# Optimization experiments

Measured on AMD Instinct MI355X. Metric: run time of the kernel, lower is better.

The kernel has to match this reference:

```python
import jax, jax.numpy as jnp
import numpy as np

NUM_NODES = 80000
NUM_EDGES = 1280000
NUM_GRAPHS = 512
IN_DIM = 64
HID = 64
NUM_CLASSES = 10


def setup_inputs() -> dict:
    key = jax.random.key(0)
    ks = jax.random.split(key, 16)
    x = jax.random.normal(ks[0], (NUM_NODES, IN_DIM), dtype=jnp.float32)
    edge_index = jax.random.randint(ks[1], (2, NUM_EDGES), 0, NUM_NODES, dtype=jnp.int64)
    batch = jnp.sort(jax.random.randint(ks[2], (NUM_NODES,), 0, NUM_GRAPHS, dtype=jnp.int64))

    def glorot(k, shape):
        fan_in, fan_out = shape[1], shape[0]
        lim = jnp.sqrt(6.0 / (fan_in + fan_out))
        return jax.random.uniform(k, shape, dtype=jnp.float32, minval=-lim, maxval=lim)

    inp = {
        "x": x,
        "edge_index": edge_index,
        "batch": batch,
        # GraphConv layer 1: lin_rel (with bias) applied to aggregated neighbors, lin_root (no bias)
        "w_rel1": glorot(ks[3], (HID, IN_DIM)),
        "b_rel1": jnp.zeros((HID,), dtype=jnp.float32),
        "w_root1": glorot(ks[4], (HID, IN_DIM)),
        # layer 2
        "w_rel2": glorot(ks[5], (HID, HID)),
        "b_rel2": jnp.zeros((HID,), dtype=jnp.float32),
        "w_root2": glorot(ks[6], (HID, HID)),
        # layer 3
        "w_rel3": glorot(ks[7], (HID, HID)),
        "b_rel3": jnp.zeros((HID,), dtype=jnp.float32),
        "w_root3": glorot(ks[8], (HID, HID)),
        # final linear head
        "w_lin": glorot(ks[9], (NUM_CLASSES, HID)),
        "b_lin": jnp.zeros((NUM_CLASSES,), dtype=jnp.float32),
    }
    return inp


def _graph_conv(x, src, dst, w_rel, b_rel, w_root):
    # PyG GraphConv with aggr='add': out_i = W_rel @ (sum_{j in N(i)} x_j) + b_rel + W_root @ x_i
    agg = jax.ops.segment_sum(x[src], dst, num_segments=NUM_NODES)  # [N, d_in]
    return agg @ w_rel.T + b_rel + x @ w_root.T


def reference(x, edge_index, batch,
              w_rel1, b_rel1, w_root1,
              w_rel2, b_rel2, w_root2,
              w_rel3, b_rel3, w_root3,
              w_lin, b_lin):
    src, dst = edge_index[0], edge_index[1]
    h = jax.nn.relu(_graph_conv(x, src, dst, w_rel1, b_rel1, w_root1))
    h = jax.nn.relu(_graph_conv(h, src, dst, w_rel2, b_rel2, w_root2))
    h = _graph_conv(h, src, dst, w_rel3, b_rel3, w_root3)
    # global_mean_pool over graph ids
    sums = jax.ops.segment_sum(h, batch, num_segments=NUM_GRAPHS)          # [G, HID]
    counts = jax.ops.segment_sum(jnp.ones((h.shape[0],), h.dtype), batch, num_segments=NUM_GRAPHS)
    pooled = sums / jnp.maximum(counts, 1.0)[:, None]
    # dropout p=0.5 is identity at inference (training=False)
    return pooled @ w_lin.T + b_lin  # [G, NUM_CLASSES]
```

## Files before the change

### kernel.cpp

```cpp
#include <hip/hip_runtime.h>

#define N_NODES  80000
#define N_EDGES  1280000
#define N_GRAPHS 512
#define DIM      64
#define NCLS     10

#define ETILE    2048
#define NTILE    625
#define NCB      313
#define CBPAD    320

typedef _Float16 half8f __attribute__((ext_vector_type(8)));
typedef float float4f __attribute__((ext_vector_type(4)));

static __device__ __forceinline__ unsigned short f2h(float f) {
    _Float16 h = (_Float16)f;
    return __builtin_bit_cast(unsigned short, h);
}
static __device__ __forceinline__ float h_lo(unsigned v) {
    return (float)__builtin_bit_cast(_Float16, (unsigned short)(v & 0xFFFF));
}
static __device__ __forceinline__ float h_hi(unsigned v) {
    return (float)__builtin_bit_cast(_Float16, (unsigned short)(v >> 16));
}

__global__ __launch_bounds__(256) void k_histprep(const int* __restrict__ ei,
        const float* __restrict__ x,
        const float* __restrict__ wr1, const float* __restrict__ wo1,
        const float* __restrict__ wr2, const float* __restrict__ wo2,
        int* __restrict__ hmat, unsigned short* __restrict__ xb,
        unsigned short* __restrict__ wf) {
    __shared__ int hist[NCB];
    int bid = blockIdx.x, t = threadIdx.x;
    if (bid < NTILE) {
        int tile = bid;
        for (int i = t; i < NCB; i += 256) hist[i] = 0;
        __syncthreads();
        int base = tile * ETILE;
        int end = base + ETILE;
        for (int i = base + t; i < end; i += 256)
            atomicAdd(&hist[ei[N_EDGES + i] >> 8], 1);
        __syncthreads();
        for (int i = t; i < NCB; i += 256) hmat[tile * CBPAD + i] = hist[i];
        return;
    }
    int pb = bid - NTILE;
    if (pb < 5000) {
        int i = pb * 256 + t;
        float4 v = ((const float4*)x)[i];
        ushort4 o;
        o.x = f2h(v.x); o.y = f2h(v.y); o.z = f2h(v.z); o.w = f2h(v.w);
        ((ushort4*)xb)[i] = o;
    } else {
        int idx = (pb - 5000) * 256 + t;
        int j = idx & 7, lane = (idx >> 3) & 63;
        int ks = (idx >> 9) & 3, nt = (idx >> 11) & 3, l = idx >> 13;
        int k = ks * 32 + ((lane >> 4) & 3) * 8 + j;
        int n = nt * 16 + (lane & 15);
        const float* wr = (l == 0) ? wr1 : wr2;
        const float* wo = (l == 0) ? wo1 : wo2;
        float val = (k < 64) ? wr[n * 64 + k] : wo[n * 64 + (k - 64)];
        wf[idx] = f2h(val);
    }
}

__global__ __launch_bounds__(256) void k_scanT(const int* __restrict__ hmat,
        int* __restrict__ obase, int* __restrict__ btot) {
    __shared__ int sa[256], sb[256];
    int b = blockIdx.x, t = threadIdx.x;
    int j0 = 3 * t;
    int l0 = (j0     < NTILE) ? hmat[(j0    ) * CBPAD + b] : 0;
    int l1 = (j0 + 1 < NTILE) ? hmat[(j0 + 1) * CBPAD + b] : 0;
    int l2 = (j0 + 2 < NTILE) ? hmat[(j0 + 2) * CBPAD + b] : 0;
    int s = l0 + l1 + l2;
    sa[t] = s; __syncthreads();
    int* sp = sa; int* dp = sb;
    for (int off = 1; off < 256; off <<= 1) {
        dp[t] = sp[t] + ((t >= off) ? sp[t - off] : 0);
        __syncthreads();
        int* tmp = sp; sp = dp; dp = tmp;
    }
    int ex = sp[t] - s;
    if (j0     < NTILE) obase[(j0    ) * CBPAD + b] = ex;
    if (j0 + 1 < NTILE) obase[(j0 + 1) * CBPAD + b] = ex + l0;
    if (j0 + 2 < NTILE) obase[(j0 + 2) * CBPAD + b] = ex + l0 + l1;
    if (t == 255) btot[b] = sp[255];
}

__global__ __launch_bounds__(256) void k_scatter2(const int* __restrict__ ei,
        const int* __restrict__ obase, const int* __restrict__ btot,
        int* __restrict__ ebuf) {
    __shared__ int sa[256], sb[256];
    __shared__ int bbase[NCB];
    __shared__ int cur[NCB];
    int tile = blockIdx.x, t = threadIdx.x;
    int l0 = (2 * t     < NCB) ? btot[2 * t]     : 0;
    int l1 = (2 * t + 1 < NCB) ? btot[2 * t + 1] : 0;
    int s = l0 + l1;
    sa[t] = s; __syncthreads();
    int* sp = sa; int* dp = sb;
    for (int off = 1; off < 256; off <<= 1) {
        dp[t] = sp[t] + ((t >= off) ? sp[t - off] : 0);
        __syncthreads();
        int* tmp = sp; sp = dp; dp = tmp;
    }
    int ex = sp[t] - s;
    if (2 * t     < NCB) bbase[2 * t]     = ex;
    if (2 * t + 1 < NCB) bbase[2 * t + 1] = ex + l0;
    __syncthreads();
    for (int i = t; i < NCB; i += 256)
        cur[i] = bbase[i] + obase[tile * CBPAD + i];
    __syncthreads();
    int base = tile * ETILE;
    int end = base + ETILE;
    for (int i = base + t; i < end; i += 256) {
        int sv = ei[i], d = ei[N_EDGES + i];
        int p = atomicAdd(&cur[d >> 8], 1);
        ebuf[p] = sv | ((d & 255) << 17);
    }
}

__global__ __launch_bounds__(256) void k_csr2(const int* __restrict__ ebuf,
        const int* __restrict__ btot, int* __restrict__ rowptr,
        int* __restrict__ col) {
    __shared__ int sa[256], sb[256];
    __shared__ int bbase[NCB];
    __shared__ int cnt[256], cur[256];
    int b = blockIdx.x, t = threadIdx.x;
    int l0 = (2 * t     < NCB) ? btot[2 * t]     : 0;
    int l1 = (2 * t + 1 < NCB) ? btot[2 * t + 1] : 0;
    int sm = l0 + l1;
    sa[t] = sm; __syncthreads();
    int* sp = sa; int* dp = sb;
    for (int off = 1; off < 256; off <<= 1) {
        dp[t] = sp[t] + ((t >= off) ? sp[t - off] : 0);
        __syncthreads();
        int* tmp = sp; sp = dp; dp = tmp;
    }
    int ex = sp[t] - sm;
    if (2 * t     < NCB) bbase[2 * t]     = ex;
    if (2 * t + 1 < NCB) bbase[2 * t + 1] = ex + l0;
    cnt[t] = 0;
    __syncthreads();
    int s = bbase[b];
    int e = s + btot[b];
    for (int i = s + t; i < e; i += 256) atomicAdd(&cnt[ebuf[i] >> 17], 1);
    __syncthreads();
    int c = cnt[t];
    sa[t] = c; __syncthreads();
    sp = sa; dp = sb;
    for (int off = 1; off < 256; off <<= 1) {
        dp[t] = sp[t] + ((t >= off) ? sp[t - off] : 0);
        __syncthreads();
        int* tmp = sp; sp = dp; dp = tmp;
    }
    int rowbase = s + sp[t] - c;
    cur[t] = rowbase;
    int node = b * 256 + t;
    if (node <= N_NODES) rowptr[node] = rowbase;
    __syncthreads();
    for (int i = s + t; i < e; i += 256) {
        int pk = ebuf[i];
        int p = atomicAdd(&cur[pk >> 17], 1);
        col[p] = pk & 0x1FFFF;
    }
}

__global__ __launch_bounds__(256) void k_gatherlin(
        const unsigned short* __restrict__ Xin,
        const int* __restrict__ rowptr, const int* __restrict__ col,
        const unsigned short* __restrict__ wf, const float* __restrict__ bias,
        unsigned short* __restrict__ out, int relu) {
    __shared__ uint4 sAgg[64][9];
    const half8f* Xq = (const half8f*)Xin;
    int t = threadIdx.x, w = t >> 6, lane = t & 63;
    int e = lane >> 3, c = lane & 7;
    int nb = blockIdx.x * 64 + w * 16;
    int rp = (lane <= 16) ? rowptr[nb + lane] : 0;
    for (int n = 0; n < 16; ++n) {
        int start = __shfl(rp, n), end = __shfl(rp, n + 1);
        half8f acc = {};
        int base = start;
        for (; base + 16 <= end; base += 16) {
            int i0 = col[base + e];
            int i1 = col[base + 8 + e];
            half8f v0 = Xq[(size_t)i0 * 8 + c];
            half8f v1 = Xq[(size_t)i1 * 8 + c];
            acc = acc + v0;
            acc = acc + v1;
        }
        for (; base + 8 <= end; base += 8) {
            int i0 = col[base + e];
            acc = acc + Xq[(size_t)i0 * 8 + c];
        }
        int r = end - base;
        if (e < r) {
            int i0 = col[base + e];
            acc = acc + Xq[(size_t)i0 * 8 + c];
        }
#pragma unroll
        for (int off = 8; off < 64; off <<= 1) {
            uint4 au = __builtin_bit_cast(uint4, acc);
            uint4 bu;
            bu.x = __shfl_xor(au.x, off); bu.y = __shfl_xor(au.y, off);
            bu.z = __shfl_xor(au.z, off); bu.w = __shfl_xor(au.w, off);
            acc = acc + __builtin_bit_cast(half8f, bu);
        }
        if (e == 0) sAgg[w * 16 + n][c] = __builtin_bit_cast(uint4, acc);
    }
    int quad = lane >> 4, l15 = lane & 15;
    int m = nb + l15;
    half8f a0 = *(const half8f*)&sAgg[w * 16 + l15][quad];
    half8f a1 = *(const half8f*)&sAgg[w * 16 + l15][4 + quad];
    const half8f* xr = (const half8f*)(Xin + (size_t)m * 64);
    half8f a2 = xr[quad];
    half8f a3 = xr[4 + quad];
    int orow = nb + quad * 4;
#pragma unroll
    for (int nt = 0; nt < 4; ++nt) {
        const half8f* wp = (const half8f*)(wf + ((size_t)(nt * 4) * 64 + lane) * 8);
        half8f b0 = wp[0];
        half8f b1 = wp[64];
        half8f b2 = wp[128];
        half8f b3 = wp[192];
        float4f acc = {0.f, 0.f, 0.f, 0.f};
        acc = __builtin_amdgcn_mfma_f32_16x16x32_f16(a0, b0, acc, 0, 0, 0);
        acc = __builtin_amdgcn_mfma_f32_16x16x32_f16(a1, b1, acc, 0, 0, 0);
        acc = __builtin_amdgcn_mfma_f32_16x16x32_f16(a2, b2, acc, 0, 0, 0);
        acc = __builtin_amdgcn_mfma_f32_16x16x32_f16(a3, b3, acc, 0, 0, 0);
        float bi = bias[nt * 16 + l15];
#pragma unroll
        for (int r = 0; r < 4; ++r) {
            float v = acc[r] + bi;
            if (relu) v = fmaxf(v, 0.f);
            out[(size_t)(orow + r) * 64 + nt * 16 + l15] = f2h(v);
        }
    }
}

static __device__ __forceinline__ int lowerb(const int* a, int n, int key) {
    int lo = 0, hi = n;
    while (lo < hi) { int mid = (lo + hi) >> 1; if (a[mid] < key) lo = mid + 1; else hi = mid; }
    return lo;
}

__global__ __launch_bounds__(256) void k_gsum(const unsigned short* __restrict__ h2,
        const int* __restrict__ rowptr, const int* __restrict__ col,
        const int* __restrict__ batch, float* __restrict__ S4) {
    __shared__ float red1[8][64];
    __shared__ float red2[8][64];
    const unsigned* Xu = (const unsigned*)h2;
    int g = blockIdx.x >> 2, part = blockIdx.x & 3;
    int t = threadIdx.x;
    int hw = t >> 5, c = t & 31;
    int ns = lowerb(batch, N_NODES, g);
    int ne = lowerb(batch, N_NODES, g + 1);
    int a0 = ns + (int)(((long long)(ne - ns) * part) >> 2);
    int a1 = ns + (int)(((long long)(ne - ns) * (part + 1)) >> 2);
    int es = rowptr[a0], ee = rowptr[a1];
    float alo = 0.f, ahi = 0.f;
    int nfull = (ee - es) >> 7;
    int e0 = es + hw * 16;
    for (int b = 0; b < nfull; ++b, e0 += 128) {
        unsigned v[16];
#pragma unroll
        for (int j = 0; j < 16; ++j)
            v[j] = Xu[(size_t)col[e0 + j] * 32 + c];
#pragma unroll
        for (int j = 0; j < 16; ++j) { alo += h_lo(v[j]); ahi += h_hi(v[j]); }
    }
    for (int e = es + nfull * 128 + hw; e < ee; e += 8) {
        unsigned v = Xu[(size_t)col[e] * 32 + c];
        alo += h_lo(v); ahi += h_hi(v);
    }
    float blo = 0.f, bhi = 0.f;
    for (int i = a0 + hw; i < a1; i += 8) {
        unsigned v = Xu[(size_t)i * 32 + c];
        blo += h_lo(v); bhi += h_hi(v);
    }
    red1[hw][2 * c] = alo; red1[hw][2 * c + 1] = ahi;
    red2[hw][2 * c] = blo; red2[hw][2 * c + 1] = bhi;
    __syncthreads();
    if (t < 64) {
        float v = 0.f;
#pragma unroll
        for (int s = 0; s < 8; ++s) v += red1[s][t];
        S4[(size_t)blockIdx.x * 128 + t] = v;
    } else if (t < 128) {
        float v = 0.f;
#pragma unroll
        for (int s = 0; s < 8; ++s) v += red2[s][t - 64];
        S4[(size_t)blockIdx.x * 128 + 64 + (t - 64)] = v;
    }
}

__global__ __launch_bounds__(64) void k_head2(const float* __restrict__ S4,
        const int* __restrict__ batch,
        const float* __restrict__ wr3, const float* __restrict__ wo3,
        const float* __restrict__ b3,
        const float* __restrict__ wlin, const float* __restrict__ blin,
        float* __restrict__ out) {
    __shared__ float s1[64], s2[64], pl[64];
    int g = blockIdx.x, t = threadIdx.x;
    int ns = lowerb(batch, N_NODES, g);
    int ne = lowerb(batch, N_NODES, g + 1);
    float inv = 1.f / (float)((ne > ns) ? (ne - ns) : 1);
    const float* Sg = S4 + (size_t)g * 4 * 128;
    s1[t] = (Sg[t]       + Sg[128 + t]       + Sg[256 + t]       + Sg[384 + t]) * inv;
    s2[t] = (Sg[64 + t]  + Sg[192 + t]       + Sg[320 + t]       + Sg[448 + t]) * inv;
    __syncthreads();
    float acc = b3[t];
    for (int k = 0; k < 64; ++k)
        acc += s1[k] * wr3[t * 64 + k] + s2[k] * wo3[t * 64 + k];
    pl[t] = acc;
    __syncthreads();
    float myout = 0.f;
    for (int cls = 0; cls < NCLS; ++cls) {
        float vv = pl[t] * wlin[cls * 64 + t];
        for (int off = 32; off > 0; off >>= 1) vv += __shfl_xor(vv, off);
        if (t == cls) myout = vv + blin[cls];
    }
    if (t < NCLS) out[g * NCLS + t] = myout;
}

extern "C" void kernel_launch(void* const* d_in, const int* in_sizes, int n_in,
                              void* d_out, int out_size, void* d_ws, size_t ws_size,
                              hipStream_t stream) {
    const float* x     = (const float*)d_in[0];
    const int*   ei    = (const int*)d_in[1];
    const int*   batch = (const int*)d_in[2];
    const float* wr1 = (const float*)d_in[3];
    const float* b1  = (const float*)d_in[4];
    const float* wo1 = (const float*)d_in[5];
    const float* wr2 = (const float*)d_in[6];
    const float* b2  = (const float*)d_in[7];
    const float* wo2 = (const float*)d_in[8];
    const float* wr3 = (const float*)d_in[9];
    const float* b3  = (const float*)d_in[10];
    const float* wo3 = (const float*)d_in[11];
    const float* wlin = (const float*)d_in[12];
    const float* blin = (const float*)d_in[13];
    float* out = (float*)d_out;

    char* p = (char*)d_ws;
    auto alloc = [&](size_t bytes) { char* r = p; p += (bytes + 255) & ~(size_t)255; return r; };
    int*   rowptr  = (int*)alloc((N_NODES + 1) * sizeof(int));
    int*   hmat    = (int*)alloc((size_t)NTILE * CBPAD * sizeof(int));
    int*   obase   = (int*)alloc((size_t)NTILE * CBPAD * sizeof(int));
    int*   btot    = (int*)alloc(CBPAD * sizeof(int));
    int*   ebuf    = (int*)alloc((size_t)N_EDGES * sizeof(int));
    int*   col     = (int*)alloc((size_t)N_EDGES * sizeof(int));
    unsigned short* wf  = (unsigned short*)alloc(2 * 8192 * sizeof(unsigned short));
    unsigned short* xbf = (unsigned short*)alloc((size_t)N_NODES * 64 * 2);
    unsigned short* hA  = (unsigned short*)alloc((size_t)N_NODES * 64 * 2);
    unsigned short* hB  = (unsigned short*)alloc((size_t)N_NODES * 64 * 2);
    float* S4      = (float*)alloc((size_t)N_GRAPHS * 4 * 128 * sizeof(float));

    k_histprep<<<NTILE + 5064, 256, 0, stream>>>(ei, x, wr1, wo1, wr2, wo2,
                                                 hmat, xbf, wf);
    k_scanT   <<<NCB,   256, 0, stream>>>(hmat, obase, btot);
    k_scatter2<<<NTILE, 256, 0, stream>>>(ei, obase, btot, ebuf);
    k_csr2    <<<NCB,   256, 0, stream>>>(ebuf, btot, rowptr, col);

    k_gatherlin<<<N_NODES / 64, 256, 0, stream>>>(xbf, rowptr, col, wf,        b1, hA, 1);
    k_gatherlin<<<N_NODES / 64, 256, 0, stream>>>(hA,  rowptr, col, wf + 8192, b2, hB, 1);

    k_gsum <<<N_GRAPHS * 4, 256, 0, stream>>>(hB, rowptr, col, batch, S4);
    k_head2<<<N_GRAPHS,     64,  0, stream>>>(S4, batch, wr3, wo3, b3, wlin, blin, out);
}
```

Before: 238.7 us.

## Use finer CSR buckets, single bucket-base scan, and vectorized gsum gathers

Bucket width for the CSR build drops from 256 to 128 nodes, so more blocks work on smaller buckets in the scan and CSR kernels. The global bucket prefix sum, which every scatter and CSR block used to recompute, now runs once in a new single-block kernel that writes bucketbase and rowptr[N]. The graph-sum kernel switches to 16-byte uint4 gathers with two loads in flight per iteration and a wave-shuffle reduction in place of 32-bit loads. The cost is one extra kernel launch and a larger histogram matrix.

```diff
diff --git a/kernel.cpp b/kernel.cpp
--- a/kernel.cpp
+++ b/kernel.cpp
@@ -8,8 +8,9 @@
 
 #define ETILE    2048
 #define NTILE    625
-#define NCB      313
-#define CBPAD    320
+#define NCB      625
+#define BSH      7
+#define HPAD     640
 
 typedef _Float16 half8f __attribute__((ext_vector_type(8)));
 typedef float float4f __attribute__((ext_vector_type(4)));
@@ -40,9 +41,9 @@
         int base = tile * ETILE;
         int end = base + ETILE;
         for (int i = base + t; i < end; i += 256)
-            atomicAdd(&hist[ei[N_EDGES + i] >> 8], 1);
-        __syncthreads();
-        for (int i = t; i < NCB; i += 256) hmat[tile * CBPAD + i] = hist[i];
+            atomicAdd(&hist[ei[N_EDGES + i] >> BSH], 1);
+        __syncthreads();
+        for (int i = t; i < NCB; i += 256) hmat[tile * HPAD + i] = hist[i];
         return;
     }
     int pb = bid - NTILE;
@@ -70,9 +71,9 @@
     __shared__ int sa[256], sb[256];
     int b = blockIdx.x, t = threadIdx.x;
     int j0 = 3 * t;
-    int l0 = (j0     < NTILE) ? hmat[(j0    ) * CBPAD + b] : 0;
-    int l1 = (j0 + 1 < NTILE) ? hmat[(j0 + 1) * CBPAD + b] : 0;
-    int l2 = (j0 + 2 < NTILE) ? hmat[(j0 + 2) * CBPAD + b] : 0;
+    int l0 = (j0     < NTILE) ? hmat[(j0    ) * HPAD + b] : 0;
+    int l1 = (j0 + 1 < NTILE) ? hmat[(j0 + 1) * HPAD + b] : 0;
+    int l2 = (j0 + 2 < NTILE) ? hmat[(j0 + 2) * HPAD + b] : 0;
     int s = l0 + l1 + l2;
     sa[t] = s; __syncthreads();
     int* sp = sa; int* dp = sb;
@@ -82,22 +83,23 @@
         int* tmp = sp; sp = dp; dp = tmp;
     }
     int ex = sp[t] - s;
-    if (j0     < NTILE) obase[(j0    ) * CBPAD + b] = ex;
-    if (j0 + 1 < NTILE) obase[(j0 + 1) * CBPAD + b] = ex + l0;
-    if (j0 + 2 < NTILE) obase[(j0 + 2) * CBPAD + b] = ex + l0 + l1;
+    if (j0     < NTILE) obase[(j0    ) * HPAD + b] = ex;
+    if (j0 + 1 < NTILE) obase[(j0 + 1) * HPAD + b] = ex + l0;
+    if (j0 + 2 < NTILE) obase[(j0 + 2) * HPAD + b] = ex + l0 + l1;
     if (t == 255) btot[b] = sp[255];
 }
 
-__global__ __launch_bounds__(256) void k_scatter2(const int* __restrict__ ei,
-        const int* __restrict__ obase, const int* __restrict__ btot,
-        int* __restrict__ ebuf) {
+__global__ __launch_bounds__(256) void k_scanB(const int* __restrict__ btot,
+        int* __restrict__ bucketbase, int* __restrict__ rowptr) {
     __shared__ int sa[256], sb[256];
-    __shared__ int bbase[NCB];
-    __shared__ int cur[NCB];
-    int tile = blockIdx.x, t = threadIdx.x;
-    int l0 = (2 * t     < NCB) ? btot[2 * t]     : 0;
-    int l1 = (2 * t + 1 < NCB) ? btot[2 * t + 1] : 0;
-    int s = l0 + l1;
+    int t = threadIdx.x;
+    int b0 = t * 5;
+    int v0 = (b0     < NCB) ? btot[b0]     : 0;
+    int v1 = (b0 + 1 < NCB) ? btot[b0 + 1] : 0;
+    int v2 = (b0 + 2 < NCB) ? btot[b0 + 2] : 0;
+    int v3 = (b0 + 3 < NCB) ? btot[b0 + 3] : 0;
+    int v4 = (b0 + 4 < NCB) ? btot[b0 + 4] : 0;
+    int s = v0 + v1 + v2 + v3 + v4;
     sa[t] = s; __syncthreads();
     int* sp = sa; int* dp = sb;
     for (int off = 1; off < 256; off <<= 1) {
@@ -106,59 +108,55 @@
         int* tmp = sp; sp = dp; dp = tmp;
     }
     int ex = sp[t] - s;
-    if (2 * t     < NCB) bbase[2 * t]     = ex;
-    if (2 * t + 1 < NCB) bbase[2 * t + 1] = ex + l0;
-    __syncthreads();
+    if (b0     < NCB) bucketbase[b0]     = ex;
+    if (b0 + 1 < NCB) bucketbase[b0 + 1] = ex + v0;
+    if (b0 + 2 < NCB) bucketbase[b0 + 2] = ex + v0 + v1;
+    if (b0 + 3 < NCB) bucketbase[b0 + 3] = ex + v0 + v1 + v2;
+    if (b0 + 4 < NCB) bucketbase[b0 + 4] = ex + v0 + v1 + v2 + v3;
+    if (t == 0) { bucketbase[NCB] = N_EDGES; rowptr[N_NODES] = N_EDGES; }
+}
+
+__global__ __launch_bounds__(256) void k_scatter2(const int* __restrict__ ei,
+        const int* __restrict__ obase, const int* __restrict__ bucketbase,
+        int* __restrict__ ebuf) {
+    __shared__ int cur[NCB];
+    int tile = blockIdx.x, t = threadIdx.x;
     for (int i = t; i < NCB; i += 256)
-        cur[i] = bbase[i] + obase[tile * CBPAD + i];
+        cur[i] = bucketbase[i] + obase[tile * HPAD + i];
     __syncthreads();
     int base = tile * ETILE;
     int end = base + ETILE;
     for (int i = base + t; i < end; i += 256) {
         int sv = ei[i], d = ei[N_EDGES + i];
-        int p = atomicAdd(&cur[d >> 8], 1);
-        ebuf[p] = sv | ((d & 255) << 17);
+        int p = atomicAdd(&cur[d >> BSH], 1);
+        ebuf[p] = sv | ((d & 127) << 17);
     }
 }
 
 __global__ __launch_bounds__(256) void k_csr2(const int* __restrict__ ebuf,
-        const int* __restrict__ btot, int* __restrict__ rowptr,
+        const int* __restrict__ bucketbase, int* __restrict__ rowptr,
         int* __restrict__ col) {
-    __shared__ int sa[256], sb[256];
-    __shared__ int bbase[NCB];
-    __shared__ int cnt[256], cur[256];
+    __shared__ int cnt[128], cur[128];
+    __shared__ int sa[128], sb[128];
     int b = blockIdx.x, t = threadIdx.x;
-    int l0 = (2 * t     < NCB) ? btot[2 * t]     : 0;
-    int l1 = (2 * t + 1 < NCB) ? btot[2 * t + 1] : 0;
-    int sm = l0 + l1;
-    sa[t] = sm; __syncthreads();
+    int s = bucketbase[b], e = bucketbase[b + 1];
+    if (t < 128) cnt[t] = 0;
+    __syncthreads();
+    for (int i = s + t; i < e; i += 256) atomicAdd(&cnt[ebuf[i] >> 17], 1);
+    __syncthreads();
+    if (t < 128) sa[t] = cnt[t];
+    __syncthreads();
     int* sp = sa; int* dp = sb;
-    for (int off = 1; off < 256; off <<= 1) {
-        dp[t] = sp[t] + ((t >= off) ? sp[t - off] : 0);
+    for (int off = 1; off < 128; off <<= 1) {
+        if (t < 128) dp[t] = sp[t] + ((t >= off) ? sp[t - off] : 0);
         __syncthreads();
         int* tmp = sp; sp = dp; dp = tmp;
     }
-    int ex = sp[t] - sm;
-    if (2 * t     < NCB) bbase[2 * t]     = ex;
-    if (2 * t + 1 < NCB) bbase[2 * t + 1] = ex + l0;
-    cnt[t] = 0;
-    __syncthreads();
-    int s = bbase[b];
-    int e = s + btot[b];
-    for (int i = s + t; i < e; i += 256) atomicAdd(&cnt[ebuf[i] >> 17], 1);
-    __syncthreads();
-    int c = cnt[t];
-    sa[t] = c; __syncthreads();
-    sp = sa; dp = sb;
-    for (int off = 1; off < 256; off <<= 1) {
-        dp[t] = sp[t] + ((t >= off) ? sp[t - off] : 0);
-        __syncthreads();
-        int* tmp = sp; sp = dp; dp = tmp;
-    }
-    int rowbase = s + sp[t] - c;
-    cur[t] = rowbase;
-    int node = b * 256 + t;
-    if (node <= N_NODES) rowptr[node] = rowbase;
+    if (t < 128) {
+        int rowbase = s + sp[t] - cnt[t];
+        cur[t] = rowbase;
+        rowptr[b * 128 + t] = rowbase;
+    }
     __syncthreads();
     for (int i = s + t; i < e; i += 256) {
         int pk = ebuf[i];
@@ -248,50 +246,68 @@
 __global__ __launch_bounds__(256) void k_gsum(const unsigned short* __restrict__ h2,
         const int* __restrict__ rowptr, const int* __restrict__ col,
         const int* __restrict__ batch, float* __restrict__ S4) {
-    __shared__ float red1[8][64];
-    __shared__ float red2[8][64];
-    const unsigned* Xu = (const unsigned*)h2;
+    __shared__ float red1[4][64];
+    __shared__ float red2[4][64];
+    const uint4* Xq = (const uint4*)h2;
     int g = blockIdx.x >> 2, part = blockIdx.x & 3;
-    int t = threadIdx.x;
-    int hw = t >> 5, c = t & 31;
+    int t = threadIdx.x, w = t >> 6, lane = t & 63;
+    int e = lane >> 3, c = lane & 7;
     int ns = lowerb(batch, N_NODES, g);
     int ne = lowerb(batch, N_NODES, g + 1);
     int a0 = ns + (int)(((long long)(ne - ns) * part) >> 2);
     int a1 = ns + (int)(((long long)(ne - ns) * (part + 1)) >> 2);
     int es = rowptr[a0], ee = rowptr[a1];
-    float alo = 0.f, ahi = 0.f;
-    int nfull = (ee - es) >> 7;
-    int e0 = es + hw * 16;
-    for (int b = 0; b < nfull; ++b, e0 += 128) {
-        unsigned v[16];
-#pragma unroll
-        for (int j = 0; j < 16; ++j)
-            v[j] = Xu[(size_t)col[e0 + j] * 32 + c];
-#pragma unroll
-        for (int j = 0; j < 16; ++j) { alo += h_lo(v[j]); ahi += h_hi(v[j]); }
-    }
-    for (int e = es + nfull * 128 + hw; e < ee; e += 8) {
-        unsigned v = Xu[(size_t)col[e] * 32 + c];
-        alo += h_lo(v); ahi += h_hi(v);
-    }
-    float blo = 0.f, bhi = 0.f;
-    for (int i = a0 + hw; i < a1; i += 8) {
-        unsigned v = Xu[(size_t)i * 32 + c];
-        blo += h_lo(v); bhi += h_hi(v);
-    }
-    red1[hw][2 * c] = alo; red1[hw][2 * c + 1] = ahi;
-    red2[hw][2 * c] = blo; red2[hw][2 * c + 1] = bhi;
+    float acc[8] = {0.f, 0.f, 0.f, 0.f, 0.f, 0.f, 0.f, 0.f};
+    int idx = es + w * 8 + e;
+    for (; idx + 32 < ee; idx += 64) {
+        int i0 = col[idx];
+        int i1 = col[idx + 32];
+        uint4 v0 = Xq[(size_t)i0 * 8 + c];
+        uint4 v1 = Xq[(size_t)i1 * 8 + c];
+        acc[0] += h_lo(v0.x) + h_lo(v1.x); acc[1] += h_hi(v0.x) + h_hi(v1.x);
+        acc[2] += h_lo(v0.y) + h_lo(v1.y); acc[3] += h_hi(v0.y) + h_hi(v1.y);
+        acc[4] += h_lo(v0.z) + h_lo(v1.z); acc[5] += h_hi(v0.z) + h_hi(v1.z);
+        acc[6] += h_lo(v0.w) + h_lo(v1.w); acc[7] += h_hi(v0.w) + h_hi(v1.w);
+    }
+    if (idx < ee) {
+        int i0 = col[idx];
+        uint4 v0 = Xq[(size_t)i0 * 8 + c];
+        acc[0] += h_lo(v0.x); acc[1] += h_hi(v0.x);
+        acc[2] += h_lo(v0.y); acc[3] += h_hi(v0.y);
+        acc[4] += h_lo(v0.z); acc[5] += h_hi(v0.z);
+        acc[6] += h_lo(v0.w); acc[7] += h_hi(v0.w);
+    }
+    float acc2[8] = {0.f, 0.f, 0.f, 0.f, 0.f, 0.f, 0.f, 0.f};
+    for (int i = a0 + w * 8 + e; i < a1; i += 32) {
+        uint4 v = Xq[(size_t)i * 8 + c];
+        acc2[0] += h_lo(v.x); acc2[1] += h_hi(v.x);
+        acc2[2] += h_lo(v.y); acc2[3] += h_hi(v.y);
+        acc2[4] += h_lo(v.z); acc2[5] += h_hi(v.z);
+        acc2[6] += h_lo(v.w); acc2[7] += h_hi(v.w);
+    }
+#pragma unroll
+    for (int off = 8; off < 64; off <<= 1) {
+#pragma unroll
+        for (int j = 0; j < 8; ++j) {
+            acc[j]  += __shfl_xor(acc[j],  off);
+            acc2[j] += __shfl_xor(acc2[j], off);
+        }
+    }
+    if (e == 0) {
+#pragma unroll
+        for (int j = 0; j < 8; ++j) {
+            red1[w][c * 8 + j] = acc[j];
+            red2[w][c * 8 + j] = acc2[j];
+        }
+    }
     __syncthreads();
     if (t < 64) {
-        float v = 0.f;
-#pragma unroll
-        for (int s = 0; s < 8; ++s) v += red1[s][t];
-        S4[(size_t)blockIdx.x * 128 + t] = v;
+        S4[(size_t)blockIdx.x * 128 + t] =
+            red1[0][t] + red1[1][t] + red1[2][t] + red1[3][t];
     } else if (t < 128) {
-        float v = 0.f;
-#pragma unroll
-        for (int s = 0; s < 8; ++s) v += red2[s][t - 64];
-        S4[(size_t)blockIdx.x * 128 + 64 + (t - 64)] = v;
+        int d = t - 64;
+        S4[(size_t)blockIdx.x * 128 + 64 + d] =
+            red2[0][d] + red2[1][d] + red2[2][d] + red2[3][d];
     }
 }
 
@@ -346,9 +362,10 @@
     char* p = (char*)d_ws;
     auto alloc = [&](size_t bytes) { char* r = p; p += (bytes + 255) & ~(size_t)255; return r; };
     int*   rowptr  = (int*)alloc((N_NODES + 1) * sizeof(int));
-    int*   hmat    = (int*)alloc((size_t)NTILE * CBPAD * sizeof(int));
-    int*   obase   = (int*)alloc((size_t)NTILE * CBPAD * sizeof(int));
-    int*   btot    = (int*)alloc(CBPAD * sizeof(int));
+    int*   hmat    = (int*)alloc((size_t)NTILE * HPAD * sizeof(int));
+    int*   obase   = (int*)alloc((size_t)NTILE * HPAD * sizeof(int));
+    int*   btot    = (int*)alloc(HPAD * sizeof(int));
+    int*   bucketbase = (int*)alloc((NCB + 1) * sizeof(int));
     int*   ebuf    = (int*)alloc((size_t)N_EDGES * sizeof(int));
     int*   col     = (int*)alloc((size_t)N_EDGES * sizeof(int));
     unsigned short* wf  = (unsigned short*)alloc(2 * 8192 * sizeof(unsigned short));
@@ -360,8 +377,9 @@
     k_histprep<<<NTILE + 5064, 256, 0, stream>>>(ei, x, wr1, wo1, wr2, wo2,
                                                  hmat, xbf, wf);
     k_scanT   <<<NCB,   256, 0, stream>>>(hmat, obase, btot);
-    k_scatter2<<<NTILE, 256, 0, stream>>>(ei, obase, btot, ebuf);
-    k_csr2    <<<NCB,   256, 0, stream>>>(ebuf, btot, rowptr, col);
+    k_scanB   <<<1,     256, 0, stream>>>(btot, bucketbase, rowptr);
+    k_scatter2<<<NTILE, 256, 0, stream>>>(ei, obase, bucketbase, ebuf);
+    k_csr2    <<<NCB,   256, 0, stream>>>(ebuf, bucketbase, rowptr, col);
 
     k_gatherlin<<<N_NODES / 64, 256, 0, stream>>>(xbf, rowptr, col, wf,        b1, hA, 1);
     k_gatherlin<<<N_NODES / 64, 256, 0, stream>>>(hA,  rowptr, col, wf + 8192, b2, hB, 1);
```

Measured after the change: 238.5 us. No clear change (-0.1%).
